# Performance work log

Hardware: AMD Instinct MI355X
Metric: run time of the kernel (lower is better)

The kernel has to match this reference:

```python
import jax, jax.numpy as jnp
import numpy as np
from jax import lax

N, C, A, K, D = 2, 256, 3, 20, 256  # batch, channels, anchors, topk person cells, rn_fc_dim
BOX = 4
SIZES = [(80, 128), (40, 64), (20, 32), (10, 16)]
DN = ('NCHW', 'OIHW', 'NCHW')


def _conv(x, w, b):
    return lax.conv_general_dilated(x, w, (1, 1), 'SAME', dimension_numbers=DN) + b[None, :, None, None]


def setup_inputs() -> dict:
    key = jax.random.key(0)
    ks = iter(jax.random.split(key, 40))
    d = {}
    for i, (h, w) in enumerate(SIZES):
        d['feat%d' % i] = jax.random.normal(next(ks), (N, C, h, w), jnp.float32)
    def wfn(shape, s=0.05):
        return jax.random.normal(next(ks), shape, jnp.float32) * s
    d['pc1_w'] = wfn((C, C, 3, 3)); d['pc1_b'] = jnp.zeros((C,), jnp.float32)
    d['pc2_w'] = wfn((C, C, 3, 3)); d['pc2_b'] = jnp.zeros((C,), jnp.float32)
    d['oc1_w'] = wfn((C, C, 3, 3)); d['oc1_b'] = jnp.zeros((C,), jnp.float32)
    d['oc2_w'] = wfn((C, C, 3, 3)); d['oc2_b'] = jnp.zeros((C,), jnp.float32)
    # relation-net FCs: first takes concat(object, person) -> 2C in
    d['rn1_w'] = wfn((D, 2 * C)); d['rn1_b'] = jnp.zeros((D,), jnp.float32)
    d['rn2_w'] = wfn((D, D)); d['rn2_b'] = jnp.zeros((D,), jnp.float32)
    # heads
    d['pl_w'] = wfn((A, C, 1, 1), 0.01); d['pl_b'] = jnp.zeros((A,), jnp.float32)
    d['pd_w'] = wfn((A * BOX, C, 1, 1), 0.01); d['pd_b'] = jnp.zeros((A * BOX,), jnp.float32)
    d['ol_w'] = wfn((A, D), 0.01); d['ol_b'] = jnp.zeros((A,), jnp.float32)
    d['od_w'] = wfn((A * BOX, C, 1, 1), 0.01); d['od_b'] = jnp.zeros((A * BOX,), jnp.float32)
    return d


def _find_top_cells(hidden, logits, topk):
    hid_l, sc_l = [], []
    for h_map, lg in zip(hidden, logits):
        n, c, H, W = h_map.shape
        cell_scores = jnp.max(lg, axis=1).reshape(n, -1)          # (N, HW)
        ts, tc = lax.top_k(cell_scores, topk)                      # (N, K)
        hv = h_map.reshape(n, c, -1)                               # (N, C, HW)
        hid_l.append(jnp.take_along_axis(hv, tc[:, None, :], axis=2))  # (N, C, K)
        sc_l.append(ts)
    scores = jnp.concatenate(sc_l, axis=1)                         # (N, L*K)
    hid = jnp.concatenate(hid_l, axis=2)                           # (N, C, L*K)
    _, keep = lax.top_k(scores, topk)
    return jnp.take_along_axis(hid, keep[:, None, :], axis=2)      # (N, C, K)


def _forward(feats, pc1_w, pc1_b, pc2_w, pc2_b, oc1_w, oc1_b, oc2_w, oc2_b,
             rn1_w, rn1_b, rn2_w, rn2_b, pl_w, pl_b, pd_w, pd_b, ol_w, ol_b, od_w, od_b):
    # person branch
    p_hid, p_log, p_del = [], [], []
    for x in feats:
        x = jax.nn.relu(_conv(x, pc1_w, pc1_b))
        x = jax.nn.relu(_conv(x, pc2_w, pc2_b))
        p_hid.append(x)
        p_log.append(_conv(x, pl_w, pl_b))
        p_del.append(_conv(x, pd_w, pd_b))
    topk_person = _find_top_cells(p_hid, p_log, K)                 # (N, C, K)
    pf = topk_person.transpose(0, 2, 1)                            # (N, K, C)
    # object branch: fc1(concat(o, p)) == o @ Wo.T + p @ Wp.T + b (concat order: object first)
    Wo, Wp = rn1_w[:, :C], rn1_w[:, C:]
    p_proj = jnp.einsum('nkc,dc->nkd', pf, Wp) + rn1_b             # (N, K, D)
    o_log, o_del = [], []
    for x in feats:
        n, _, H, W = x.shape
        y = jax.nn.relu(_conv(x, oc1_w, oc1_b))
        y = jax.nn.relu(_conv(y, oc2_w, oc2_b))
        o_del.append(_conv(y, od_w, od_b))
        yf = y.reshape(n, C, H * W).transpose(0, 2, 1)             # (N, HW, C)
        o_proj = jnp.einsum('nsc,dc->nsd', yf, Wo)                 # (N, HW, D)
        h = jax.nn.relu(o_proj[:, :, None, :] + p_proj[:, None, :, :])  # (N, HW, K, D)
        h = h.sum(axis=2)                                          # (N, HW, D)
        h = jax.nn.relu(jnp.einsum('nsd,ed->nse', h, rn2_w) + rn2_b)
        ol = jnp.einsum('nsd,ad->nsa', h, ol_w) + ol_b             # (N, HW, A)
        o_log.append(ol.transpose(0, 2, 1).reshape(n, A, H, W))
    return tuple(p_log) + tuple(p_del) + tuple(o_log) + tuple(o_del)


def reference(feat0, feat1, feat2, feat3, pc1_w, pc1_b, pc2_w, pc2_b, oc1_w, oc1_b, oc2_w, oc2_b,
              rn1_w, rn1_b, rn2_w, rn2_b, pl_w, pl_b, pd_w, pd_b, ol_w, ol_b, od_w, od_b):
    return _forward([feat0, feat1, feat2, feat3], pc1_w, pc1_b, pc2_w, pc2_b, oc1_w, oc1_b,
                    oc2_w, oc2_b, rn1_w, rn1_b, rn2_w, rn2_b, pl_w, pl_b, pd_w, pd_b,
                    ol_w, ol_b, od_w, od_b)
```

## Files before the change

kernel.cpp:

```cpp
#include <hip/hip_runtime.h>
#include <cstdint>
#include <cstddef>

typedef __bf16 bf16x8 __attribute__((ext_vector_type(8)));
typedef float  f32x16 __attribute__((ext_vector_type(16)));

union U16 { bf16x8 v; uint4 q; };
union U8  { __bf16 h[4]; unsigned long long u; };

typedef __attribute__((address_space(1))) const unsigned char gas_t;
typedef __attribute__((address_space(3))) unsigned char las_t;
__device__ __forceinline__ void async16(const void* g, void* l) {
    __builtin_amdgcn_global_load_lds((gas_t*)g, (las_t*)l, 16, 0, 0);
}

__device__ __forceinline__ int lvl256(int bx) {
    return (bx < 40) ? 0 : (bx < 50) ? 1 : (bx < 53) ? 2 : 3;
}
__device__ __forceinline__ int tbase256(int lv) {
    return (lv == 0) ? 0 : (lv == 1) ? 40 : (lv == 2) ? 50 : 53;
}
__device__ __forceinline__ size_t loffE(int lv) {
    return (lv == 0) ? 0 : (lv == 1) ? 5242880 : (lv == 2) ? 6553600 : 6881280;
}
__device__ __forceinline__ size_t plog_off(int lv) {
    return (lv == 0) ? 0 : (lv == 1) ? 61440 : (lv == 2) ? 76800 : 80640;
}
__device__ __forceinline__ size_t pdel_off(int lv) {
    return (lv == 0) ? 81600 : (lv == 1) ? 327360 : (lv == 2) ? 388800 : 404160;
}
__device__ __forceinline__ size_t olog_off(int lv) {
    return (lv == 0) ? 408000 : (lv == 1) ? 469440 : (lv == 2) ? 484800 : 488640;
}
__device__ __forceinline__ size_t odel_off(int lv) {
    return (lv == 0) ? 489600 : (lv == 1) ? 735360 : (lv == 2) ? 796800 : 812160;
}
__device__ __forceinline__ int soff_l(int lv) {
    return (lv == 0) ? 0 : (lv == 1) ? 20480 : (lv == 2) ? 25600 : 26880;
}

__global__ __launch_bounds__(256) void prep_all_k(
    const float* f0, const float* f1, const float* f2, const float* f3,
    const float* pc1w, const float* pc2w, const float* oc1w, const float* oc2w,
    const float* __restrict__ rn1w, const float* __restrict__ rn2w,
    __bf16* __restrict__ wtap, float* __restrict__ WpT,
    __bf16* __restrict__ Wo16, __bf16* __restrict__ rn216,
    unsigned* __restrict__ zrow32, __bf16* __restrict__ x16)
{
    int bid = blockIdx.x, tid = threadIdx.x;
    if (bid < 576) {
        int which = bid / 144, r = bid - which * 144, t = r >> 4, c16 = r & 15;
        const float* src = (which == 0) ? pc1w : (which == 1) ? pc2w
                         : (which == 2) ? oc1w : oc2w;
        __bf16* dst = wtap + (size_t)which * 589824;
        int co = tid, cg = co >> 6, co64 = co & 63;
        U16 a, b;
#pragma unroll
        for (int j = 0; j < 8; ++j)
            a.v[j] = (__bf16)src[(size_t)(co * 256 + c16 * 16 + j) * 9 + t];
#pragma unroll
        for (int j = 0; j < 8; ++j)
            b.v[j] = (__bf16)src[(size_t)(co * 256 + c16 * 16 + 8 + j) * 9 + t];
        size_t base = (size_t)t * 65536 + (size_t)c16 * 4096 + (size_t)cg * 1024 + co64 * 8;
        *(uint4*)&dst[base] = a.q;
        *(uint4*)&dst[base + 512] = b.q;
    } else if (bid < 832) {
        int d = bid - 576, c = tid;
        WpT[c * 256 + d] = rn1w[(size_t)d * 512 + 256 + c];
        Wo16[((c >> 4) * 256 + d) * 16 + (c & 15)] = (__bf16)rn1w[(size_t)d * 512 + c];
        rn216[((c >> 4) * 256 + d) * 16 + (c & 15)] = (__bf16)rn2w[(size_t)d * 256 + c];
        if (d == 0) zrow32[c] = 0u;
    } else {
        int u = bid - 832;
        int bx = u >> 5, rr = u & 31, n = rr >> 4, ch = rr & 15;
        int lv = lvl256(bx);
        int HW = 10240 >> (2 * lv);
        int p = (bx - tbase256(lv)) * 256 + tid;
        if (p >= HW) return;
        const float* f = (lv == 0) ? f0 : (lv == 1) ? f1 : (lv == 2) ? f2 : f3;
        const float* src = f + (size_t)n * 256 * HW + (size_t)ch * 16 * HW + p;
        U16 a, b;
#pragma unroll
        for (int j = 0; j < 8; ++j) a.v[j] = (__bf16)src[(size_t)j * HW];
#pragma unroll
        for (int j = 0; j < 8; ++j) b.v[j] = (__bf16)src[(size_t)(8 + j) * HW];
        size_t o = loffE(lv) + (size_t)n * HW * 256 + (((size_t)ch * HW + p) << 4);
        *(uint4*)&x16[o] = a.q;
        *(uint4*)&x16[o + 8] = b.q;
    }
}

__global__ __launch_bounds__(256) void conv3x3_v5(
    const __bf16* __restrict__ inA, const __bf16* __restrict__ inB,
    const __bf16* __restrict__ wtA, const __bf16* __restrict__ wtB,
    const float* __restrict__ bA, const float* __restrict__ bB,
    const __bf16* __restrict__ zrow,
    __bf16* __restrict__ outA, __bf16* __restrict__ outB)
{
    __shared__ __bf16 Asm[2][9216];

    const int tid = threadIdx.x;
    const int zz = blockIdx.z;
    const int n = zz & 1, br = (zz >> 1) & 1;
    const __bf16* in16 = br ? inB : inA;
    const __bf16* wt = br ? wtB : wtA;
    const float* bias = br ? bB : bA;
    __bf16* outp = br ? outB : outA;

    const int bx = blockIdx.x;
    const int lv = lvl256(bx);
    const int lg2W = 7 - lv;
    const int W = 1 << lg2W, H = 80 >> lv;
    const int HW = 10240 >> (2 * lv);
    const size_t ioff = loffE(lv) + (size_t)n * HW * 256;
    const __bf16* inb = in16 + ioff;

    const int tile = bx - tbase256(lv);
    const int sp0 = tile << 8;
    const int npix = min(256, HW - sp0);

    const int w = tid >> 6, l64 = tid & 63;
    const int lane = l64 & 31, half = l64 >> 5;
    const int pix0 = (w << 6) + lane, pix1 = pix0 + 32;
    const int cobase = blockIdx.y << 6;

    int boff0[9], boff1[9];
    {
        const int y0 = sp0 >> lg2W;
        const int py0 = pix0 >> lg2W, px0 = pix0 & (W - 1);
        const int py1 = pix1 >> lg2W, px1 = pix1 & (W - 1);
#pragma unroll
        for (int dy = 0; dy < 3; ++dy)
#pragma unroll
            for (int dx = 0; dx < 3; ++dx) {
                int t = dy * 3 + dx;
                int gy0 = y0 + py0 + dy - 1, gx0 = px0 + dx - 1;
                boff0[t] = ((unsigned)gy0 < (unsigned)H && (unsigned)gx0 < (unsigned)W)
                           ? (((gy0 << lg2W) + gx0) * 32 + half * 16) : -1;
                int gy1 = y0 + py1 + dy - 1, gx1 = px1 + dx - 1;
                boff1[t] = ((unsigned)gy1 < (unsigned)H && (unsigned)gx1 < (unsigned)W)
                           ? (((gy1 << lg2W) + gx1) * 32 + half * 16) : -1;
            }
    }
    const __bf16* zp = zrow + (half << 3);

    const char* wtb = (const char*)wt + (blockIdx.y * 2048);
    auto stage = [&](int c16, int buf) {
        const char* base = wtb + (size_t)c16 * 8192;
        for (int u = w; u < 18; u += 4) {
            int t = u >> 1, hf = u & 1;
            async16(base + (size_t)t * 131072 + hf * 1024 + l64 * 16,
                    &Asm[buf][u * 512]);
        }
    };

    f32x16 acc00 = {}, acc01 = {}, acc10 = {}, acc11 = {};

    stage(0, 0);
    int buf = 0;
    for (int c16 = 0; c16 < 16; ++c16) {
        __syncthreads();
        if (c16 < 15) stage(c16 + 1, buf ^ 1);
        const char* curB = (const char*)inb + (size_t)c16 * HW * 32;
        const __bf16* Ab = &Asm[buf][0];
#pragma unroll
        for (int t = 0; t < 9; ++t) {
            bf16x8 a0 = *(const bf16x8*)&Ab[t * 1024 + half * 512 + lane * 8];
            bf16x8 a1 = *(const bf16x8*)&Ab[t * 1024 + half * 512 + 256 + lane * 8];
            const __bf16* q0 = (boff0[t] >= 0) ? (const __bf16*)(curB + boff0[t]) : zp;
            const __bf16* q1 = (boff1[t] >= 0) ? (const __bf16*)(curB + boff1[t]) : zp;
            bf16x8 b0 = *(const bf16x8*)q0;
            bf16x8 b1 = *(const bf16x8*)q1;
            acc00 = __builtin_amdgcn_mfma_f32_32x32x16_bf16(a0, b0, acc00, 0, 0, 0);
            acc01 = __builtin_amdgcn_mfma_f32_32x32x16_bf16(a0, b1, acc01, 0, 0, 0);
            acc10 = __builtin_amdgcn_mfma_f32_32x32x16_bf16(a1, b0, acc10, 0, 0, 0);
            acc11 = __builtin_amdgcn_mfma_f32_32x32x16_bf16(a1, b1, acc11, 0, 0, 0);
        }
        buf ^= 1;
    }
    const int pixg0 = sp0 + pix0, pixg1 = sp0 + pix1;
    const bool ok0 = (pix0 < npix), ok1 = (pix1 < npix);
#pragma unroll
    for (int b = 0; b < 2; ++b) {
        const f32x16& A0 = b ? acc10 : acc00;
        const f32x16& A1 = b ? acc11 : acc01;
#pragma unroll
        for (int q = 0; q < 4; ++q) {
            int co0 = cobase + b * 32 + q * 8 + half * 4;
            float4 bq = *(const float4*)&bias[co0];
            U8 v0, v1;
            v0.h[0] = (__bf16)fmaxf(A0[q * 4 + 0] + bq.x, 0.f);
            v0.h[1] = (__bf16)fmaxf(A0[q * 4 + 1] + bq.y, 0.f);
            v0.h[2] = (__bf16)fmaxf(A0[q * 4 + 2] + bq.z, 0.f);
            v0.h[3] = (__bf16)fmaxf(A0[q * 4 + 3] + bq.w, 0.f);
            v1.h[0] = (__bf16)fmaxf(A1[q * 4 + 0] + bq.x, 0.f);
            v1.h[1] = (__bf16)fmaxf(A1[q * 4 + 1] + bq.y, 0.f);
            v1.h[2] = (__bf16)fmaxf(A1[q * 4 + 2] + bq.z, 0.f);
            v1.h[3] = (__bf16)fmaxf(A1[q * 4 + 3] + bq.w, 0.f);
            size_t base = ioff + (((size_t)(co0 >> 4) * HW) << 4) + (co0 & 15);
            if (ok0) *(unsigned long long*)&outp[base + ((size_t)pixg0 << 4)] = v0.u;
            if (ok1) *(unsigned long long*)&outp[base + ((size_t)pixg1 << 4)] = v1.u;
        }
    }
}

__global__ __launch_bounds__(256) void heads_k(
    const __bf16* __restrict__ h16p, const __bf16* __restrict__ h16o,
    const float* __restrict__ plw, const float* __restrict__ plb,
    const float* __restrict__ pdw, const float* __restrict__ pdb,
    const float* __restrict__ odw, const float* __restrict__ odb,
    float* __restrict__ out, float* __restrict__ scores)
{
    int bx = blockIdx.x, n = blockIdx.y, br = blockIdx.z;
    int lv = lvl256(bx);
    int HW = 10240 >> (2 * lv);
    int p = (bx - tbase256(lv)) * 256 + threadIdx.x;
    if (p >= HW) return;
    size_t ioff = loffE(lv) + (size_t)n * HW * 256;
    if (br == 0) {
        float acc[15];
#pragma unroll
        for (int a = 0; a < 15; ++a) acc[a] = 0.f;
        for (int ch = 0; ch < 16; ++ch) {
            size_t base = ioff + (((size_t)ch * HW + p) << 4);
            bf16x8 v0 = *(const bf16x8*)&h16p[base];
            bf16x8 v1 = *(const bf16x8*)&h16p[base + 8];
#pragma unroll
            for (int j = 0; j < 16; ++j) {
                float vv = (j < 8) ? (float)v0[j] : (float)v1[j - 8];
                int c = ch * 16 + j;
#pragma unroll
                for (int a = 0; a < 3; ++a)  acc[a]     = fmaf(plw[a * 256 + c], vv, acc[a]);
#pragma unroll
                for (int a = 0; a < 12; ++a) acc[3 + a] = fmaf(pdw[a * 256 + c], vv, acc[3 + a]);
            }
        }
        float sc = -INFINITY;
#pragma unroll
        for (int a = 0; a < 3; ++a) {
            float lg = acc[a] + plb[a];
            out[plog_off(lv) + ((size_t)n * 3 + a) * HW + p] = lg;
            sc = fmaxf(sc, lg);
        }
        scores[soff_l(lv) + (size_t)n * HW + p] = sc;
#pragma unroll
        for (int a = 0; a < 12; ++a)
            out[pdel_off(lv) + ((size_t)n * 12 + a) * HW + p] = acc[3 + a] + pdb[a];
    } else {
        float acc[12];
#pragma unroll
        for (int a = 0; a < 12; ++a) acc[a] = 0.f;
        for (int ch = 0; ch < 16; ++ch) {
            size_t base = ioff + (((size_t)ch * HW + p) << 4);
            bf16x8 v0 = *(const bf16x8*)&h16o[base];
            bf16x8 v1 = *(const bf16x8*)&h16o[base + 8];
#pragma unroll
            for (int j = 0; j < 16; ++j) {
                float vv = (j < 8) ? (float)v0[j] : (float)v1[j - 8];
                int c = ch * 16 + j;
#pragma unroll
                for (int a = 0; a < 12; ++a) acc[a] = fmaf(odw[a * 256 + c], vv, acc[a]);
            }
        }
#pragma unroll
        for (int a = 0; a < 12; ++a)
            out[odel_off(lv) + ((size_t)n * 12 + a) * HW + p] = acc[a] + odb[a];
    }
}

__global__ __launch_bounds__(256) void topk_lvl_k(
    const float* __restrict__ scores, float* __restrict__ lv_sc,
    int* __restrict__ lv_ix)
{
    int l = blockIdx.x, n = blockIdx.y;
    int HW = 10240 >> (2 * l);
    const float* sp = scores + soff_l(l) + (size_t)n * HW;
    int tid = threadIdx.x;
    __shared__ float sc[10240];
    __shared__ float wv4[4];
    __shared__ int wi4[4];
    __shared__ int bcast;
    for (int i = tid; i < HW; i += 256) sc[i] = sp[i];
    __syncthreads();
    float bv = -INFINITY; int bi = 0x7fffffff;
    for (int i = tid; i < HW; i += 256)
        if (sc[i] > bv) { bv = sc[i]; bi = i; }
    const int w = tid >> 6, lane = tid & 63;
    for (int r = 0; r < 20; ++r) {
        float cv = bv; int ci = bi;
#pragma unroll
        for (int off = 32; off > 0; off >>= 1) {
            float ov = __shfl_xor(cv, off);
            int oi = __shfl_xor(ci, off);
            if (ov > cv || (ov == cv && oi < ci)) { cv = ov; ci = oi; }
        }
        if (lane == 0) { wv4[w] = cv; wi4[w] = ci; }
        __syncthreads();
        if (tid == 0) {
            float mv = wv4[0]; int mi = wi4[0];
#pragma unroll
            for (int j = 1; j < 4; ++j)
                if (wv4[j] > mv || (wv4[j] == mv && wi4[j] < mi)) { mv = wv4[j]; mi = wi4[j]; }
            bcast = mi;
            int idx = (n * 4 + l) * 20 + r;
            lv_sc[idx] = mv;
            lv_ix[idx] = mi;
        }
        __syncthreads();
        int mi = bcast;
        if ((mi & 255) == tid) {
            sc[mi] = -INFINITY;
            bv = -INFINITY; bi = 0x7fffffff;
            for (int i = tid; i < HW; i += 256)
                if (sc[i] > bv) { bv = sc[i]; bi = i; }
        }
    }
}

__global__ __launch_bounds__(256) void sel_pproj_k(
    const float* __restrict__ lv_sc, const int* __restrict__ lv_ix,
    const __bf16* __restrict__ h16p, const float* __restrict__ WpT,
    const float* __restrict__ rn1b, float* __restrict__ pp)
{
    int n = blockIdx.x, tid = threadIdx.x;
    __shared__ int selL[20], selC[20];
    __shared__ float pfL[5120];
    __shared__ float wv2[2];
    __shared__ int wi2[2];
    __shared__ int bcast;
    float bv = -INFINITY; int bi = 0x7fffffff;
    if (tid < 80) { bv = lv_sc[n * 80 + tid]; bi = tid; }
    const int w = tid >> 6, lane = tid & 63;
    for (int r = 0; r < 20; ++r) {
        float cv = bv; int ci = bi;
#pragma unroll
        for (int off = 32; off > 0; off >>= 1) {
            float ov = __shfl_xor(cv, off);
            int oi = __shfl_xor(ci, off);
            if (ov > cv || (ov == cv && oi < ci)) { cv = ov; ci = oi; }
        }
        if (lane == 0 && w < 2) { wv2[w] = cv; wi2[w] = ci; }
        __syncthreads();
        if (tid == 0) {
            float mv = wv2[0]; int mi = wi2[0];
            if (wv2[1] > mv || (wv2[1] == mv && wi2[1] < mi)) { mv = wv2[1]; mi = wi2[1]; }
            bcast = mi;
            selL[r] = mi / 20;
            selC[r] = lv_ix[n * 80 + mi];
        }
        __syncthreads();
        if (bcast == bi) bv = -INFINITY;
    }
    for (int t = tid; t < 5120; t += 256) {
        int k = t >> 8, c = t & 255;
        int l = selL[k], cell = selC[k];
        int HW = 10240 >> (2 * l);
        pfL[k * 256 + c] =
            (float)h16p[loffE(l) + (size_t)n * HW * 256 +
                        (((size_t)(c >> 4) * HW + cell) << 4) + (c & 15)];
    }
    __syncthreads();
    float acc[20];
    float bb = rn1b[tid];
#pragma unroll
    for (int k = 0; k < 20; ++k) acc[k] = bb;
    for (int c = 0; c < 256; ++c) {
        float wv = WpT[c * 256 + tid];
#pragma unroll
        for (int k = 0; k < 20; ++k) acc[k] = fmaf(pfL[k * 256 + c], wv, acc[k]);
    }
#pragma unroll
    for (int k = 0; k < 20; ++k)
        pp[(size_t)n * 5120 + k * 256 + tid] = acc[k];
}

__global__ __launch_bounds__(256) void orel_k(
    const __bf16* __restrict__ H16o, const __bf16* __restrict__ Wo16,
    const __bf16* __restrict__ rn216, const float* __restrict__ pp,
    const float* __restrict__ rn2b, const float* __restrict__ olw,
    const float* __restrict__ olb, float* __restrict__ out)
{
    __shared__ __bf16 hb[16 * 64 * 24];
    __shared__ __bf16 pp16[5120];
    const int tid = threadIdx.x;
    const int n = blockIdx.y;
    int bx = blockIdx.x;
    int lv = (bx < 160) ? 0 : (bx < 200) ? 1 : (bx < 210) ? 2 : 3;
    int tb = (lv == 0) ? 0 : (lv == 1) ? 160 : (lv == 2) ? 200 : 210;
    int HW = 10240 >> (2 * lv);
    size_t yoff = loffE(lv) + (size_t)n * HW * 256;
    int p0 = (bx - tb) << 6;
    int npix = min(64, HW - p0);

    {
        const float* ps = pp + (size_t)n * 5120;
        for (int i = tid; i < 1280; i += 256) {
            float4 f = *(const float4*)&ps[i * 4];
            U8 v;
            v.h[0] = (__bf16)f.x; v.h[1] = (__bf16)f.y;
            v.h[2] = (__bf16)f.z; v.h[3] = (__bf16)f.w;
            *(unsigned long long*)&pp16[i * 4] = v.u;
        }
    }
    __syncthreads();

    const int w = tid >> 6, l64 = tid & 63;
    const int lane = l64 & 31, half = l64 >> 5;
    const int dbase = w << 6;

    f32x16 acc00 = {}, acc01 = {}, acc10 = {}, acc11 = {};
    for (int c16 = 0; c16 < 16; ++c16) {
        bf16x8 a0 = *(const bf16x8*)&Wo16[(((c16 << 8) + dbase + lane) << 4) + (half << 3)];
        bf16x8 a1 = *(const bf16x8*)&Wo16[(((c16 << 8) + dbase + 32 + lane) << 4) + (half << 3)];
        bf16x8 b0 = *(const bf16x8*)&H16o[yoff + (((size_t)c16 * HW + p0 + lane) << 4) + (half << 3)];
        bf16x8 b1 = *(const bf16x8*)&H16o[yoff + (((size_t)c16 * HW + p0 + 32 + lane) << 4) + (half << 3)];
        acc00 = __builtin_amdgcn_mfma_f32_32x32x16_bf16(a0, b0, acc00, 0, 0, 0);
        acc01 = __builtin_amdgcn_mfma_f32_32x32x16_bf16(a0, b1, acc01, 0, 0, 0);
        acc10 = __builtin_amdgcn_mfma_f32_32x32x16_bf16(a1, b0, acc10, 0, 0, 0);
        acc11 = __builtin_amdgcn_mfma_f32_32x32x16_bf16(a1, b1, acc11, 0, 0, 0);
    }
#pragma unroll
    for (int b = 0; b < 2; ++b) {
        const f32x16& A0 = b ? acc10 : acc00;
        const f32x16& A1 = b ? acc11 : acc01;
#pragma unroll
        for (int q = 0; q < 4; ++q) {
            int d0 = dbase + b * 32 + q * 8 + half * 4;
            float h0[4] = {0.f, 0.f, 0.f, 0.f}, h1[4] = {0.f, 0.f, 0.f, 0.f};
            for (int k = 0; k < 20; ++k) {
                U8 pk;
                pk.u = *(const unsigned long long*)&pp16[k * 256 + d0];
#pragma unroll
                for (int j = 0; j < 4; ++j) {
                    float pkv = (float)pk.h[j];
                    h0[j] += fmaxf(A0[q * 4 + j] + pkv, 0.f);
                    h1[j] += fmaxf(A1[q * 4 + j] + pkv, 0.f);
                }
            }
            U8 v0, v1;
#pragma unroll
            for (int j = 0; j < 4; ++j) { v0.h[j] = (__bf16)h0[j]; v1.h[j] = (__bf16)h1[j]; }
            *(unsigned long long*)&hb[((d0 >> 4) * 64 + lane) * 24 + (d0 & 15)] = v0.u;
            *(unsigned long long*)&hb[((d0 >> 4) * 64 + 32 + lane) * 24 + (d0 & 15)] = v1.u;
        }
    }
    __syncthreads();
    f32x16 e00 = {}, e01 = {}, e10 = {}, e11 = {};
    for (int d16 = 0; d16 < 16; ++d16) {
        bf16x8 a0 = *(const bf16x8*)&rn216[(((d16 << 8) + dbase + lane) << 4) + (half << 3)];
        bf16x8 a1 = *(const bf16x8*)&rn216[(((d16 << 8) + dbase + 32 + lane) << 4) + (half << 3)];
        bf16x8 b0 = *(const bf16x8*)&hb[(d16 * 64 + lane) * 24 + (half << 3)];
        bf16x8 b1 = *(const bf16x8*)&hb[(d16 * 64 + 32 + lane) * 24 + (half << 3)];
        e00 = __builtin_amdgcn_mfma_f32_32x32x16_bf16(a0, b0, e00, 0, 0, 0);
        e01 = __builtin_amdgcn_mfma_f32_32x32x16_bf16(a0, b1, e01, 0, 0, 0);
        e10 = __builtin_amdgcn_mfma_f32_32x32x16_bf16(a1, b0, e10, 0, 0, 0);
        e11 = __builtin_amdgcn_mfma_f32_32x32x16_bf16(a1, b1, e11, 0, 0, 0);
    }
    __syncthreads();
#pragma unroll
    for (int b = 0; b < 2; ++b) {
        const f32x16& A0 = b ? e10 : e00;
        const f32x16& A1 = b ? e11 : e01;
#pragma unroll
        for (int q = 0; q < 4; ++q) {
            int e0 = dbase + b * 32 + q * 8 + half * 4;
            float4 bb = *(const float4*)&rn2b[e0];
            U8 v0, v1;
            v0.h[0] = (__bf16)fmaxf(A0[q * 4 + 0] + bb.x, 0.f);
            v0.h[1] = (__bf16)fmaxf(A0[q * 4 + 1] + bb.y, 0.f);
            v0.h[2] = (__bf16)fmaxf(A0[q * 4 + 2] + bb.z, 0.f);
            v0.h[3] = (__bf16)fmaxf(A0[q * 4 + 3] + bb.w, 0.f);
            v1.h[0] = (__bf16)fmaxf(A1[q * 4 + 0] + bb.x, 0.f);
            v1.h[1] = (__bf16)fmaxf(A1[q * 4 + 1] + bb.y, 0.f);
            v1.h[2] = (__bf16)fmaxf(A1[q * 4 + 2] + bb.z, 0.f);
            v1.h[3] = (__bf16)fmaxf(A1[q * 4 + 3] + bb.w, 0.f);
            *(unsigned long long*)&hb[((e0 >> 4) * 64 + lane) * 24 + (e0 & 15)] = v0.u;
            *(unsigned long long*)&hb[((e0 >> 4) * 64 + 32 + lane) * 24 + (e0 & 15)] = v1.u;
        }
    }
    __syncthreads();
    if (tid < 192) {
        int px = tid / 3, a = tid - px * 3;
        if (px < npix) {
            float s = olb[a];
            for (int e = 0; e < 256; ++e)
                s = fmaf(olw[a * 256 + e], (float)hb[((e >> 4) * 64 + px) * 24 + (e & 15)], s);
            out[olog_off(lv) + ((size_t)n * 3 + a) * HW + p0 + px] = s;
        }
    }
}

extern "C" void kernel_launch(void* const* d_in, const int* in_sizes, int n_in,
                              void* d_out, int out_size, void* d_ws, size_t ws_size,
                              hipStream_t stream)
{
    const float* feat[4] = {(const float*)d_in[0], (const float*)d_in[1],
                            (const float*)d_in[2], (const float*)d_in[3]};
    const float* pc1w = (const float*)d_in[4];  const float* pc1b = (const float*)d_in[5];
    const float* pc2w = (const float*)d_in[6];  const float* pc2b = (const float*)d_in[7];
    const float* oc1w = (const float*)d_in[8];  const float* oc1b = (const float*)d_in[9];
    const float* oc2w = (const float*)d_in[10]; const float* oc2b = (const float*)d_in[11];
    const float* rn1w = (const float*)d_in[12]; const float* rn1b = (const float*)d_in[13];
    const float* rn2w = (const float*)d_in[14]; const float* rn2b = (const float*)d_in[15];
    const float* plw  = (const float*)d_in[16]; const float* plb  = (const float*)d_in[17];
    const float* pdw  = (const float*)d_in[18]; const float* pdb  = (const float*)d_in[19];
    const float* olw  = (const float*)d_in[20]; const float* olb  = (const float*)d_in[21];
    const float* odw  = (const float*)d_in[22]; const float* odb  = (const float*)d_in[23];

    float* ws = (float*)d_ws;
    __bf16* bufA = (__bf16*)(ws);
    __bf16* bufB = (__bf16*)(ws + 3481600);
    __bf16* bufC = (__bf16*)(ws + 6963200);
    __bf16* wtap = (__bf16*)(ws + 10444800);
    __bf16* wt_pc1 = wtap;
    __bf16* wt_pc2 = wtap + 589824;
    __bf16* wt_oc1 = wtap + 2 * 589824;
    __bf16* wt_oc2 = wtap + 3 * 589824;
    __bf16* Wo16  = (__bf16*)(ws + 11624448);
    __bf16* rn216 = (__bf16*)(ws + 11657216);
    float* WpT    = ws + 11689984;
    float* scores = ws + 11755520;
    float* lv_sc  = ws + 11783040;
    int*   lv_ix  = (int*)(ws + 11783200);
    float* pp     = ws + 11793280;
    __bf16* zrow  = (__bf16*)(ws + 11803520);
    __bf16* bufD  = (__bf16*)(ws + 11803904);
    float* out    = (float*)d_out;

    const bool merged = ws_size >= (size_t)(11803904 + 3481600) * 4;

    hipLaunchKernelGGL(prep_all_k, dim3(2560), dim3(256), 0, stream,
                       feat[0], feat[1], feat[2], feat[3],
                       pc1w, pc2w, oc1w, oc2w, rn1w, rn2w,
                       wtap, WpT, Wo16, rn216, (unsigned*)zrow, bufA);

    hipLaunchKernelGGL(conv3x3_v5, dim3(54, 4, 4), dim3(256), 0, stream,
                       bufA, bufA, wt_pc1, wt_oc1, pc1b, oc1b, zrow, bufB, bufC);

    __bf16* h16o;
    if (merged) {
        hipLaunchKernelGGL(conv3x3_v5, dim3(54, 4, 4), dim3(256), 0, stream,
                           bufB, bufC, wt_pc2, wt_oc2, pc2b, oc2b, zrow, bufA, bufD);
        h16o = bufD;
    } else {
        hipLaunchKernelGGL(conv3x3_v5, dim3(54, 4, 2), dim3(256), 0, stream,
                           bufB, bufB, wt_pc2, wt_pc2, pc2b, pc2b, zrow, bufA, bufA);
        hipLaunchKernelGGL(conv3x3_v5, dim3(54, 4, 2), dim3(256), 0, stream,
                           bufC, bufC, wt_oc2, wt_oc2, oc2b, oc2b, zrow, bufB, bufB);
        h16o = bufB;
    }

    hipLaunchKernelGGL(heads_k, dim3(54, 2, 2), dim3(256), 0, stream,
                       bufA, h16o, plw, plb, pdw, pdb, odw, odb, out, scores);

    hipLaunchKernelGGL(topk_lvl_k, dim3(4, 2), dim3(256), 0, stream,
                       scores, lv_sc, lv_ix);
    hipLaunchKernelGGL(sel_pproj_k, dim3(2), dim3(256), 0, stream,
                       lv_sc, lv_ix, bufA, WpT, rn1b, pp);

    hipLaunchKernelGGL(orel_k, dim3(213, 2), dim3(256), 0, stream,
                       h16o, Wo16, rn216, pp, rn2b, olw, olb, out);
}
```

Before: 537.1 us.

## Remap conv grid for XCD-aware scheduling, stage weight repack in LDS, MFMA the object-logit head

The conv kernels now take a flattened 1D grid and remap block ids in groups of 8. Blocks that share the same input tile and weights should then land on the same XCD, which should improve L2 reuse. Weight repacking now loads each output channel's 2304 floats into LDS with coalesced reads, replacing strided global gathers. The object-logit dot product in orel_k becomes an MFMA against a padded bf16 copy of ol_w, followed by a shared-memory reduction, replacing a scalar 256-step loop per pixel. The trade-offs are bf16 rounding in the logit head and a more complex block index mapping.

```diff
diff --git a/kernel.cpp b/kernel.cpp
--- a/kernel.cpp
+++ b/kernel.cpp
@@ -43,42 +43,46 @@
     const float* f0, const float* f1, const float* f2, const float* f3,
     const float* pc1w, const float* pc2w, const float* oc1w, const float* oc2w,
     const float* __restrict__ rn1w, const float* __restrict__ rn2w,
+    const float* __restrict__ olw,
     __bf16* __restrict__ wtap, float* __restrict__ WpT,
     __bf16* __restrict__ Wo16, __bf16* __restrict__ rn216,
+    __bf16* __restrict__ olw32,
     unsigned* __restrict__ zrow32, __bf16* __restrict__ x16)
 {
+    __shared__ float f[2304];
     int bid = blockIdx.x, tid = threadIdx.x;
-    if (bid < 576) {
-        int which = bid / 144, r = bid - which * 144, t = r >> 4, c16 = r & 15;
-        const float* src = (which == 0) ? pc1w : (which == 1) ? pc2w
-                         : (which == 2) ? oc1w : oc2w;
+    if (bid < 1024) {
+        int which = bid >> 8, co = bid & 255;
+        const float* srcw = (which == 0) ? pc1w : (which == 1) ? pc2w
+                          : (which == 2) ? oc1w : oc2w;
+        const float* src = srcw + (size_t)co * 2304;
+        for (int i = tid; i < 2304; i += 256) f[i] = src[i];
+        __syncthreads();
         __bf16* dst = wtap + (size_t)which * 589824;
-        int co = tid, cg = co >> 6, co64 = co & 63;
-        U16 a, b;
-#pragma unroll
-        for (int j = 0; j < 8; ++j)
-            a.v[j] = (__bf16)src[(size_t)(co * 256 + c16 * 16 + j) * 9 + t];
-#pragma unroll
-        for (int j = 0; j < 8; ++j)
-            b.v[j] = (__bf16)src[(size_t)(co * 256 + c16 * 16 + 8 + j) * 9 + t];
-        size_t base = (size_t)t * 65536 + (size_t)c16 * 4096 + (size_t)cg * 1024 + co64 * 8;
-        *(uint4*)&dst[base] = a.q;
-        *(uint4*)&dst[base + 512] = b.q;
-    } else if (bid < 832) {
-        int d = bid - 576, c = tid;
+        int cg = co >> 6, co64 = co & 63;
+        for (int u = tid; u < 288; u += 256) {
+            int t = u >> 5, rest = u & 31, c16 = rest >> 1, hf = rest & 1;
+            int ci0 = c16 * 16 + hf * 8;
+            U16 v;
+#pragma unroll
+            for (int j = 0; j < 8; ++j) v.v[j] = (__bf16)f[(ci0 + j) * 9 + t];
+            *(uint4*)&dst[(size_t)t * 65536 + c16 * 4096 + cg * 1024 + hf * 512 + co64 * 8] = v.q;
+        }
+    } else if (bid < 1280) {
+        int d = bid - 1024, c = tid;
         WpT[c * 256 + d] = rn1w[(size_t)d * 512 + 256 + c];
         Wo16[((c >> 4) * 256 + d) * 16 + (c & 15)] = (__bf16)rn1w[(size_t)d * 512 + c];
         rn216[((c >> 4) * 256 + d) * 16 + (c & 15)] = (__bf16)rn2w[(size_t)d * 256 + c];
         if (d == 0) zrow32[c] = 0u;
-    } else {
-        int u = bid - 832;
+    } else if (bid < 3008) {
+        int u = bid - 1280;
         int bx = u >> 5, rr = u & 31, n = rr >> 4, ch = rr & 15;
         int lv = lvl256(bx);
         int HW = 10240 >> (2 * lv);
         int p = (bx - tbase256(lv)) * 256 + tid;
         if (p >= HW) return;
-        const float* f = (lv == 0) ? f0 : (lv == 1) ? f1 : (lv == 2) ? f2 : f3;
-        const float* src = f + (size_t)n * 256 * HW + (size_t)ch * 16 * HW + p;
+        const float* fp = (lv == 0) ? f0 : (lv == 1) ? f1 : (lv == 2) ? f2 : f3;
+        const float* src = fp + (size_t)n * 256 * HW + (size_t)ch * 16 * HW + p;
         U16 a, b;
 #pragma unroll
         for (int j = 0; j < 8; ++j) a.v[j] = (__bf16)src[(size_t)j * HW];
@@ -87,42 +91,62 @@
         size_t o = loffE(lv) + (size_t)n * HW * 256 + (((size_t)ch * HW + p) << 4);
         *(uint4*)&x16[o] = a.q;
         *(uint4*)&x16[o + 8] = b.q;
-    }
-}
-
-__global__ __launch_bounds__(256) void conv3x3_v5(
+    } else {
+        int e16 = bid - 3008;
+        for (int idx = tid; idx < 512; idx += 256) {
+            int co = idx >> 4, j = idx & 15;
+            float v = (co < 3) ? olw[co * 256 + e16 * 16 + j] : 0.f;
+            olw32[e16 * 512 + co * 16 + j] = (__bf16)v;
+        }
+    }
+}
+
+__global__ __launch_bounds__(256) void conv3x3_v6(
     const __bf16* __restrict__ inA, const __bf16* __restrict__ inB,
     const __bf16* __restrict__ wtA, const __bf16* __restrict__ wtB,
     const float* __restrict__ bA, const float* __restrict__ bB,
     const __bf16* __restrict__ zrow,
-    __bf16* __restrict__ outA, __bf16* __restrict__ outB)
+    __bf16* __restrict__ outA, __bf16* __restrict__ outB, int mode)
 {
     __shared__ __bf16 Asm[2][9216];
 
+    const int id = blockIdx.x;
+    const int r8 = id & 7, q = id >> 3;
+    int by, br, n, tile;
+    if (mode == 0) {
+        by = q & 3; br = (q >> 2) & 1;
+        int T = ((q >> 3) << 3) + r8; if (T >= 108) return;
+        n = T & 1; tile = T >> 1;
+    } else if (mode == 1) {
+        by = q & 3;
+        int T2 = ((q >> 2) << 3) + r8; if (T2 >= 216) return;
+        br = T2 & 1; n = (T2 >> 1) & 1; tile = T2 >> 2;
+    } else {
+        by = q & 3; br = 0;
+        int T = ((q >> 2) << 3) + r8; if (T >= 108) return;
+        n = T & 1; tile = T >> 1;
+    }
+
     const int tid = threadIdx.x;
-    const int zz = blockIdx.z;
-    const int n = zz & 1, br = (zz >> 1) & 1;
     const __bf16* in16 = br ? inB : inA;
     const __bf16* wt = br ? wtB : wtA;
     const float* bias = br ? bB : bA;
     __bf16* outp = br ? outB : outA;
 
-    const int bx = blockIdx.x;
-    const int lv = lvl256(bx);
+    const int lv = lvl256(tile);
     const int lg2W = 7 - lv;
     const int W = 1 << lg2W, H = 80 >> lv;
     const int HW = 10240 >> (2 * lv);
     const size_t ioff = loffE(lv) + (size_t)n * HW * 256;
     const __bf16* inb = in16 + ioff;
 
-    const int tile = bx - tbase256(lv);
-    const int sp0 = tile << 8;
+    const int sp0 = (tile - tbase256(lv)) << 8;
     const int npix = min(256, HW - sp0);
 
     const int w = tid >> 6, l64 = tid & 63;
     const int lane = l64 & 31, half = l64 >> 5;
     const int pix0 = (w << 6) + lane, pix1 = pix0 + 32;
-    const int cobase = blockIdx.y << 6;
+    const int cobase = by << 6;
 
     int boff0[9], boff1[9];
     {
@@ -144,7 +168,7 @@
     }
     const __bf16* zp = zrow + (half << 3);
 
-    const char* wtb = (const char*)wt + (blockIdx.y * 2048);
+    const char* wtb = (const char*)wt + (by * 2048);
     auto stage = [&](int c16, int buf) {
         const char* base = wtb + (size_t)c16 * 8192;
         for (int u = w; u < 18; u += 4) {
@@ -185,18 +209,18 @@
         const f32x16& A0 = b ? acc10 : acc00;
         const f32x16& A1 = b ? acc11 : acc01;
 #pragma unroll
-        for (int q = 0; q < 4; ++q) {
-            int co0 = cobase + b * 32 + q * 8 + half * 4;
+        for (int qq = 0; qq < 4; ++qq) {
+            int co0 = cobase + b * 32 + qq * 8 + half * 4;
             float4 bq = *(const float4*)&bias[co0];
             U8 v0, v1;
-            v0.h[0] = (__bf16)fmaxf(A0[q * 4 + 0] + bq.x, 0.f);
-            v0.h[1] = (__bf16)fmaxf(A0[q * 4 + 1] + bq.y, 0.f);
-            v0.h[2] = (__bf16)fmaxf(A0[q * 4 + 2] + bq.z, 0.f);
-            v0.h[3] = (__bf16)fmaxf(A0[q * 4 + 3] + bq.w, 0.f);
-            v1.h[0] = (__bf16)fmaxf(A1[q * 4 + 0] + bq.x, 0.f);
-            v1.h[1] = (__bf16)fmaxf(A1[q * 4 + 1] + bq.y, 0.f);
-            v1.h[2] = (__bf16)fmaxf(A1[q * 4 + 2] + bq.z, 0.f);
-            v1.h[3] = (__bf16)fmaxf(A1[q * 4 + 3] + bq.w, 0.f);
+            v0.h[0] = (__bf16)fmaxf(A0[qq * 4 + 0] + bq.x, 0.f);
+            v0.h[1] = (__bf16)fmaxf(A0[qq * 4 + 1] + bq.y, 0.f);
+            v0.h[2] = (__bf16)fmaxf(A0[qq * 4 + 2] + bq.z, 0.f);
+            v0.h[3] = (__bf16)fmaxf(A0[qq * 4 + 3] + bq.w, 0.f);
+            v1.h[0] = (__bf16)fmaxf(A1[qq * 4 + 0] + bq.x, 0.f);
+            v1.h[1] = (__bf16)fmaxf(A1[qq * 4 + 1] + bq.y, 0.f);
+            v1.h[2] = (__bf16)fmaxf(A1[qq * 4 + 2] + bq.z, 0.f);
+            v1.h[3] = (__bf16)fmaxf(A1[qq * 4 + 3] + bq.w, 0.f);
             size_t base = ioff + (((size_t)(co0 >> 4) * HW) << 4) + (co0 & 15);
             if (ok0) *(unsigned long long*)&outp[base + ((size_t)pixg0 << 4)] = v0.u;
             if (ok1) *(unsigned long long*)&outp[base + ((size_t)pixg1 << 4)] = v1.u;
@@ -376,12 +400,13 @@
 
 __global__ __launch_bounds__(256) void orel_k(
     const __bf16* __restrict__ H16o, const __bf16* __restrict__ Wo16,
-    const __bf16* __restrict__ rn216, const float* __restrict__ pp,
-    const float* __restrict__ rn2b, const float* __restrict__ olw,
+    const __bf16* __restrict__ rn216, const __bf16* __restrict__ olw32,
+    const float* __restrict__ pp, const float* __restrict__ rn2b,
     const float* __restrict__ olb, float* __restrict__ out)
 {
     __shared__ __bf16 hb[16 * 64 * 24];
     __shared__ __bf16 pp16[5120];
+    __shared__ float red[768];
     const int tid = threadIdx.x;
     const int n = blockIdx.y;
     int bx = blockIdx.x;
@@ -479,13 +504,30 @@
         }
     }
     __syncthreads();
+    f32x16 ol0 = {}, ol1 = {};
+#pragma unroll
+    for (int j = 0; j < 4; ++j) {
+        int e16 = w * 4 + j;
+        bf16x8 a = *(const bf16x8*)&olw32[e16 * 512 + lane * 16 + (half << 3)];
+        bf16x8 b0 = *(const bf16x8*)&hb[(e16 * 64 + lane) * 24 + (half << 3)];
+        bf16x8 b1 = *(const bf16x8*)&hb[(e16 * 64 + 32 + lane) * 24 + (half << 3)];
+        ol0 = __builtin_amdgcn_mfma_f32_32x32x16_bf16(a, b0, ol0, 0, 0, 0);
+        ol1 = __builtin_amdgcn_mfma_f32_32x32x16_bf16(a, b1, ol1, 0, 0, 0);
+    }
+    if (half == 0) {
+#pragma unroll
+        for (int r = 0; r < 3; ++r) {
+            red[(r * 64 + lane) * 4 + w] = ol0[r];
+            red[(r * 64 + lane + 32) * 4 + w] = ol1[r];
+        }
+    }
+    __syncthreads();
     if (tid < 192) {
-        int px = tid / 3, a = tid - px * 3;
+        int a = tid >> 6, px = tid & 63;
         if (px < npix) {
-            float s = olb[a];
-            for (int e = 0; e < 256; ++e)
-                s = fmaf(olw[a * 256 + e], (float)hb[((e >> 4) * 64 + px) * 24 + (e & 15)], s);
-            out[olog_off(lv) + ((size_t)n * 3 + a) * HW + p0 + px] = s;
+            float4 p4 = *(const float4*)&red[(a * 64 + px) * 4];
+            out[olog_off(lv) + ((size_t)n * 3 + a) * HW + p0 + px] =
+                olb[a] + p4.x + p4.y + p4.z + p4.w;
         }
     }
 }
@@ -522,6 +564,7 @@
     float* scores = ws + 11755520;
     float* lv_sc  = ws + 11783040;
     int*   lv_ix  = (int*)(ws + 11783200);
+    __bf16* olw32 = (__bf16*)(ws + 11783360);
     float* pp     = ws + 11793280;
     __bf16* zrow  = (__bf16*)(ws + 11803520);
     __bf16* bufD  = (__bf16*)(ws + 11803904);
@@ -529,24 +572,28 @@
 
     const bool merged = ws_size >= (size_t)(11803904 + 3481600) * 4;
 
-    hipLaunchKernelGGL(prep_all_k, dim3(2560), dim3(256), 0, stream,
+    hipLaunchKernelGGL(prep_all_k, dim3(3024), dim3(256), 0, stream,
                        feat[0], feat[1], feat[2], feat[3],
-                       pc1w, pc2w, oc1w, oc2w, rn1w, rn2w,
-                       wtap, WpT, Wo16, rn216, (unsigned*)zrow, bufA);
-
-    hipLaunchKernelGGL(conv3x3_v5, dim3(54, 4, 4), dim3(256), 0, stream,
-                       bufA, bufA, wt_pc1, wt_oc1, pc1b, oc1b, zrow, bufB, bufC);
+                       pc1w, pc2w, oc1w, oc2w, rn1w, rn2w, olw,
+                       wtap, WpT, Wo16, rn216, olw32, (unsigned*)zrow, bufA);
+
+    hipLaunchKernelGGL(conv3x3_v6, dim3(896), dim3(256), 0, stream,
+                       bufA, bufA, wt_pc1, wt_oc1, pc1b, oc1b, zrow,
+                       bufB, bufC, 0);
 
     __bf16* h16o;
     if (merged) {
-        hipLaunchKernelGGL(conv3x3_v5, dim3(54, 4, 4), dim3(256), 0, stream,
-                           bufB, bufC, wt_pc2, wt_oc2, pc2b, oc2b, zrow, bufA, bufD);
+        hipLaunchKernelGGL(conv3x3_v6, dim3(864), dim3(256), 0, stream,
+                           bufB, bufC, wt_pc2, wt_oc2, pc2b, oc2b, zrow,
+                           bufA, bufD, 1);
         h16o = bufD;
     } else {
-        hipLaunchKernelGGL(conv3x3_v5, dim3(54, 4, 2), dim3(256), 0, stream,
-                           bufB, bufB, wt_pc2, wt_pc2, pc2b, pc2b, zrow, bufA, bufA);
-        hipLaunchKernelGGL(conv3x3_v5, dim3(54, 4, 2), dim3(256), 0, stream,
-                           bufC, bufC, wt_oc2, wt_oc2, oc2b, oc2b, zrow, bufB, bufB);
+        hipLaunchKernelGGL(conv3x3_v6, dim3(448), dim3(256), 0, stream,
+                           bufB, bufB, wt_pc2, wt_pc2, pc2b, pc2b, zrow,
+                           bufA, bufA, 2);
+        hipLaunchKernelGGL(conv3x3_v6, dim3(448), dim3(256), 0, stream,
+                           bufC, bufC, wt_oc2, wt_oc2, oc2b, oc2b, zrow,
+                           bufB, bufB, 2);
         h16o = bufB;
     }
 
@@ -559,5 +606,5 @@
                        lv_sc, lv_ix, bufA, WpT, rn1b, pp);
 
     hipLaunchKernelGGL(orel_k, dim3(213, 2), dim3(256), 0, stream,
-                       h16o, Wo16, rn216, pp, rn2b, olw, olb, out);
-}
+                       h16o, Wo16, rn216, olw32, pp, rn2b, olb, out);
+}
```

Result: faster. 510.4 us (-5.0%).
